# Optimization experiments

Measured on AMD Instinct MI355X. Metric: run time of the kernel, lower is better.

## Reference

```python
import jax, jax.numpy as jnp
import numpy as np

D = 768
OUT = 196
EPS = 1e-6


def setup_inputs() -> dict:
    key = jax.random.key(0)
    k_x, k_w, k_b, k_g, k_beta = jax.random.split(key, 5)
    x = jax.random.normal(k_x, (16, 4096, D), dtype=jnp.float32)
    # LayerNorm affine params
    gamma = jnp.ones((D,), dtype=jnp.float32) + 0.01 * jax.random.normal(k_g, (D,), dtype=jnp.float32)
    beta = 0.01 * jax.random.normal(k_beta, (D,), dtype=jnp.float32)
    # Linear params (torch default init: U(-1/sqrt(D), 1/sqrt(D)))
    bound = 1.0 / np.sqrt(D)
    W = jax.random.uniform(k_w, (OUT, D), minval=-bound, maxval=bound, dtype=jnp.float32)
    b = jax.random.uniform(k_b, (OUT,), minval=-bound, maxval=bound, dtype=jnp.float32)
    return {"x": x, "gamma": gamma, "beta": beta, "W": W, "b": b}


def reference(x, gamma, beta, W, b):
    # LayerNorm over last dim (768), eps=1e-6, elementwise affine
    mean = jnp.mean(x, axis=-1, keepdims=True)
    var = jnp.mean(jnp.square(x - mean), axis=-1, keepdims=True)
    xn = (x - mean) * jax.lax.rsqrt(var + EPS) * gamma + beta
    # Linear 768 -> 196
    return jnp.einsum('bsd,od->bso', xn, W) + b
```

## Files before the change

### kernel.cpp

```cpp
#include <hip/hip_runtime.h>

#define DD    768
#define OUTN  196
#define MT    16
#define KC    256
#define APAD  264
#define KTS   8

typedef __attribute__((ext_vector_type(8))) _Float16 halfx8;
typedef __attribute__((ext_vector_type(4))) _Float16 halfx4;
typedef __attribute__((ext_vector_type(4))) float    f32x4;

__global__ __launch_bounds__(256) void wprep_kernel(const float4* __restrict__ W4,
                                                    halfx4* __restrict__ Wh4) {
    int i = blockIdx.x * 256 + threadIdx.x;
    if (i < OUTN * DD / 4) {
        float4 v = W4[i];
        halfx4 h;
        h[0] = (_Float16)v.x; h[1] = (_Float16)v.y;
        h[2] = (_Float16)v.z; h[3] = (_Float16)v.w;
        Wh4[i] = h;
    }
}

__global__ __launch_bounds__(256, 4) void fused_ln_linear(
    const float* __restrict__ x, const float* __restrict__ gamma,
    const float* __restrict__ beta, const _Float16* __restrict__ Wh,
    const float* __restrict__ bias, float* __restrict__ out)
{
    __shared__ _Float16 Ahi[2][MT * APAD];
    __shared__ _Float16 Alo[2][MT * APAD];

    const int tid  = threadIdx.x;
    const int wv   = tid >> 6;
    const int lane = tid & 63;
    const long row0 = (long)blockIdx.x * MT;
    const float* xrow = x + (row0 + wv * 4) * DD + lane * 4;

    float mean[4], rstd[4];
    {
        float s[4], ss[4];
#pragma unroll
        for (int t = 0; t < 4; ++t) { s[t] = 0.f; ss[t] = 0.f; }
#pragma unroll
        for (int t = 0; t < 4; ++t) {
#pragma unroll
            for (int c = 0; c < 3; ++c) {
                const float4 v = *(const float4*)(xrow + t * DD + c * KC);
                s[t]  += v.x + v.y + v.z + v.w;
                ss[t] += v.x * v.x + v.y * v.y + v.z * v.z + v.w * v.w;
            }
        }
#pragma unroll
        for (int t = 0; t < 4; ++t) {
#pragma unroll
            for (int off = 32; off > 0; off >>= 1) {
                s[t]  += __shfl_xor(s[t],  off);
                ss[t] += __shfl_xor(ss[t], off);
            }
            mean[t] = s[t] * (1.f / DD);
            const float var = ss[t] * (1.f / DD) - mean[t] * mean[t];
            rstd[t] = rsqrtf(var + 1e-6f);
        }
    }

    const int cnt  = (wv == 0) ? 4 : 3;
    const int nt0  = (wv == 0) ? 0 : (1 + 3 * wv);
    const int ln16 = lane & 15;
    const int q    = lane >> 4;

    int ncol[4], nload[4];
    float bs[4];
#pragma unroll
    for (int i = 0; i < 4; ++i) {
        const int n = (nt0 + i) * 16 + ln16;
        ncol[i]  = n;
        nload[i] = (n < OUTN ? n : OUTN - 1) * DD;
        bs[i]    = (n < OUTN) ? bias[n] : 0.f;
    }

    f32x4 acc[4];
#pragma unroll
    for (int i = 0; i < 4; ++i) acc[i] = (f32x4){0.f, 0.f, 0.f, 0.f};

    auto stage_write = [&](int st, int buf) {
        const int k0 = st * KC + lane * 4;
        const float4 gv = *(const float4*)(gamma + k0);
        const float4 bv = *(const float4*)(beta + k0);
#pragma unroll
        for (int t = 0; t < 4; ++t) {
            const float4 v = *(const float4*)(xrow + t * DD + st * KC);
            const float y0 = (v.x - mean[t]) * rstd[t] * gv.x + bv.x;
            const float y1 = (v.y - mean[t]) * rstd[t] * gv.y + bv.y;
            const float y2 = (v.z - mean[t]) * rstd[t] * gv.z + bv.z;
            const float y3 = (v.w - mean[t]) * rstd[t] * gv.w + bv.w;
            halfx4 hi, lo;
            hi[0] = (_Float16)y0; lo[0] = (_Float16)(y0 - (float)hi[0]);
            hi[1] = (_Float16)y1; lo[1] = (_Float16)(y1 - (float)hi[1]);
            hi[2] = (_Float16)y2; lo[2] = (_Float16)(y2 - (float)hi[2]);
            hi[3] = (_Float16)y3; lo[3] = (_Float16)(y3 - (float)hi[3]);
            const int r = wv * 4 + t;
            *(halfx4*)(&Ahi[buf][r * APAD + lane * 4]) = hi;
            *(halfx4*)(&Alo[buf][r * APAD + lane * 4]) = lo;
        }
    };

    auto gemm_stage = [&](int st, int buf) {
        const _Float16* Aph = &Ahi[buf][ln16 * APAD + q * 8];
        const _Float16* Apl = &Alo[buf][ln16 * APAD + q * 8];
#pragma unroll
        for (int kt = 0; kt < KTS; ++kt) {
            const halfx8 ah = *(const halfx8*)(Aph + kt * 32);
            const halfx8 al = *(const halfx8*)(Apl + kt * 32);
#pragma unroll
            for (int i = 0; i < 4; ++i) {
                if (i < cnt) {
                    const halfx8 bf =
                        *(const halfx8*)(Wh + nload[i] + st * KC + kt * 32 + q * 8);
                    acc[i] = __builtin_amdgcn_mfma_f32_16x16x32_f16(ah, bf, acc[i], 0, 0, 0);
                    acc[i] = __builtin_amdgcn_mfma_f32_16x16x32_f16(al, bf, acc[i], 0, 0, 0);
                }
            }
        }
    };

    stage_write(0, 0);
    __syncthreads();

    stage_write(1, 1);
    gemm_stage(0, 0);
    __syncthreads();

    stage_write(2, 0);
    gemm_stage(1, 1);
    __syncthreads();

    gemm_stage(2, 0);

    const long rbase = row0 + q * 4;
#pragma unroll
    for (int i = 0; i < 4; ++i) {
        if (i < cnt && ncol[i] < OUTN) {
#pragma unroll
            for (int rg = 0; rg < 4; ++rg)
                out[(rbase + rg) * OUTN + ncol[i]] = acc[i][rg] + bs[i];
        }
    }
}

extern "C" void kernel_launch(void* const* d_in, const int* in_sizes, int n_in,
                              void* d_out, int out_size, void* d_ws, size_t ws_size,
                              hipStream_t stream) {
    const float* x     = (const float*)d_in[0];
    const float* gamma = (const float*)d_in[1];
    const float* beta  = (const float*)d_in[2];
    const float* W     = (const float*)d_in[3];
    const float* b     = (const float*)d_in[4];
    float* out = (float*)d_out;
    _Float16* Wh = (_Float16*)d_ws;

    wprep_kernel<<<(OUTN * DD / 4 + 255) / 256, 256, 0, stream>>>(
        (const float4*)W, (halfx4*)Wh);

    const long rows = 16L * 4096;
    fused_ln_linear<<<rows / MT, 256, 0, stream>>>(x, gamma, beta, Wh, b, out);
}
```

Before: 416.0 us.

## Fold LayerNorm affine into weights and apply normalization after GEMM

Gamma is folded into the fp16 weights, and beta·W plus the bias is precomputed into a per-output constant. The main kernel then multiplies raw x (split into hi/lo fp16) directly and applies mean/rstd as an epilogue correction using per-column weight sums. This removes the separate statistics pass, the LDS staging and the block barriers, and lets each wave own 16 rows across all 13 output tiles straight from registers. The cost is heavy register pressure from 13 accumulators. It also risks precision loss from cancellation in acc - mean*Ssum, and the weight sum is taken over fp16-rounded weights times fp32 x.

```diff
diff --git a/kernel.cpp b/kernel.cpp
--- a/kernel.cpp
+++ b/kernel.cpp
@@ -1,149 +1,119 @@
 #include <hip/hip_runtime.h>
 
-#define DD    768
-#define OUTN  196
-#define MT    16
-#define KC    256
-#define APAD  264
-#define KTS   8
+#define DD   768
+#define OUTN 196
+#define NT   13
+#define KT   24
 
 typedef __attribute__((ext_vector_type(8))) _Float16 halfx8;
-typedef __attribute__((ext_vector_type(4))) _Float16 halfx4;
 typedef __attribute__((ext_vector_type(4))) float    f32x4;
 
-__global__ __launch_bounds__(256) void wprep_kernel(const float4* __restrict__ W4,
-                                                    halfx4* __restrict__ Wh4) {
-    int i = blockIdx.x * 256 + threadIdx.x;
-    if (i < OUTN * DD / 4) {
-        float4 v = W4[i];
-        halfx4 h;
-        h[0] = (_Float16)v.x; h[1] = (_Float16)v.y;
-        h[2] = (_Float16)v.z; h[3] = (_Float16)v.w;
-        Wh4[i] = h;
+__global__ __launch_bounds__(256) void wprep_kernel(
+    const float* __restrict__ W, const float* __restrict__ gamma,
+    const float* __restrict__ beta, const float* __restrict__ bias,
+    _Float16* __restrict__ Wh, float* __restrict__ Ssum, float* __restrict__ cvec)
+{
+    __shared__ float red[2][4];
+    const int n   = blockIdx.x;
+    const int tid = threadIdx.x;
+    float s1 = 0.f, s2 = 0.f;
+#pragma unroll
+    for (int kk = 0; kk < 3; ++kk) {
+        const int k = tid + kk * 256;
+        const float w = W[n * DD + k];
+        const _Float16 h = (_Float16)(w * gamma[k]);
+        Wh[n * DD + k] = h;
+        s1 += (float)h;
+        s2 += beta[k] * w;
+    }
+#pragma unroll
+    for (int off = 32; off > 0; off >>= 1) {
+        s1 += __shfl_xor(s1, off);
+        s2 += __shfl_xor(s2, off);
+    }
+    if ((tid & 63) == 0) { red[0][tid >> 6] = s1; red[1][tid >> 6] = s2; }
+    __syncthreads();
+    if (tid == 0) {
+        Ssum[n] = red[0][0] + red[0][1] + red[0][2] + red[0][3];
+        cvec[n] = bias[n] + red[1][0] + red[1][1] + red[1][2] + red[1][3];
     }
 }
 
 __global__ __launch_bounds__(256, 4) void fused_ln_linear(
-    const float* __restrict__ x, const float* __restrict__ gamma,
-    const float* __restrict__ beta, const _Float16* __restrict__ Wh,
-    const float* __restrict__ bias, float* __restrict__ out)
+    const float* __restrict__ x, const _Float16* __restrict__ Wh,
+    const float* __restrict__ Ssum, const float* __restrict__ cvec,
+    float* __restrict__ out)
 {
-    __shared__ _Float16 Ahi[2][MT * APAD];
-    __shared__ _Float16 Alo[2][MT * APAD];
-
     const int tid  = threadIdx.x;
     const int wv   = tid >> 6;
     const int lane = tid & 63;
-    const long row0 = (long)blockIdx.x * MT;
-    const float* xrow = x + (row0 + wv * 4) * DD + lane * 4;
+    const int ln16 = lane & 15;
+    const int q    = lane >> 4;
 
-    float mean[4], rstd[4];
-    {
-        float s[4], ss[4];
+    const long row0 = (long)blockIdx.x * 64 + wv * 16;
+    const float* xp = x + (row0 + ln16) * DD + q * 8;
+
+    int woff[NT];
 #pragma unroll
-        for (int t = 0; t < 4; ++t) { s[t] = 0.f; ss[t] = 0.f; }
+    for (int nt = 0; nt < NT; ++nt) {
+        int n = nt * 16 + ln16;
+        if (n >= OUTN) n = OUTN - 1;
+        woff[nt] = n * DD + q * 8;
+    }
+
+    f32x4 acc[NT];
 #pragma unroll
-        for (int t = 0; t < 4; ++t) {
+    for (int i = 0; i < NT; ++i) acc[i] = (f32x4){0.f, 0.f, 0.f, 0.f};
+
+    float s = 0.f, ss = 0.f;
+
+#pragma unroll 2
+    for (int kt = 0; kt < KT; ++kt) {
+        const float4 v0 = *(const float4*)(xp + kt * 32);
+        const float4 v1 = *(const float4*)(xp + kt * 32 + 4);
+        s  += v0.x + v0.y + v0.z + v0.w + v1.x + v1.y + v1.z + v1.w;
+        ss += v0.x * v0.x + v0.y * v0.y + v0.z * v0.z + v0.w * v0.w
+            + v1.x * v1.x + v1.y * v1.y + v1.z * v1.z + v1.w * v1.w;
+        halfx8 hi, lo;
+        hi[0] = (_Float16)v0.x; lo[0] = (_Float16)(v0.x - (float)hi[0]);
+        hi[1] = (_Float16)v0.y; lo[1] = (_Float16)(v0.y - (float)hi[1]);
+        hi[2] = (_Float16)v0.z; lo[2] = (_Float16)(v0.z - (float)hi[2]);
+        hi[3] = (_Float16)v0.w; lo[3] = (_Float16)(v0.w - (float)hi[3]);
+        hi[4] = (_Float16)v1.x; lo[4] = (_Float16)(v1.x - (float)hi[4]);
+        hi[5] = (_Float16)v1.y; lo[5] = (_Float16)(v1.y - (float)hi[5]);
+        hi[6] = (_Float16)v1.z; lo[6] = (_Float16)(v1.z - (float)hi[6]);
+        hi[7] = (_Float16)v1.w; lo[7] = (_Float16)(v1.w - (float)hi[7]);
 #pragma unroll
-            for (int c = 0; c < 3; ++c) {
-                const float4 v = *(const float4*)(xrow + t * DD + c * KC);
-                s[t]  += v.x + v.y + v.z + v.w;
-                ss[t] += v.x * v.x + v.y * v.y + v.z * v.z + v.w * v.w;
-            }
-        }
-#pragma unroll
-        for (int t = 0; t < 4; ++t) {
-#pragma unroll
-            for (int off = 32; off > 0; off >>= 1) {
-                s[t]  += __shfl_xor(s[t],  off);
-                ss[t] += __shfl_xor(ss[t], off);
-            }
-            mean[t] = s[t] * (1.f / DD);
-            const float var = ss[t] * (1.f / DD) - mean[t] * mean[t];
-            rstd[t] = rsqrtf(var + 1e-6f);
+        for (int nt = 0; nt < NT; ++nt) {
+            const halfx8 bw = *(const halfx8*)(Wh + woff[nt] + kt * 32);
+            acc[nt] = __builtin_amdgcn_mfma_f32_16x16x32_f16(hi, bw, acc[nt], 0, 0, 0);
+            acc[nt] = __builtin_amdgcn_mfma_f32_16x16x32_f16(lo, bw, acc[nt], 0, 0, 0);
         }
     }
 
-    const int cnt  = (wv == 0) ? 4 : 3;
-    const int nt0  = (wv == 0) ? 0 : (1 + 3 * wv);
-    const int ln16 = lane & 15;
-    const int q    = lane >> 4;
+    s  += __shfl_xor(s, 16);  s  += __shfl_xor(s, 32);
+    ss += __shfl_xor(ss, 16); ss += __shfl_xor(ss, 32);
+    const float mean_r = s * (1.f / DD);
+    const float rstd_r = rsqrtf(ss * (1.f / DD) - mean_r * mean_r + 1e-6f);
 
-    int ncol[4], nload[4];
-    float bs[4];
+    float mb[4], rb[4];
 #pragma unroll
-    for (int i = 0; i < 4; ++i) {
-        const int n = (nt0 + i) * 16 + ln16;
-        ncol[i]  = n;
-        nload[i] = (n < OUTN ? n : OUTN - 1) * DD;
-        bs[i]    = (n < OUTN) ? bias[n] : 0.f;
+    for (int rg = 0; rg < 4; ++rg) {
+        const int src = q * 4 + rg;
+        mb[rg] = __shfl(mean_r, src);
+        rb[rg] = __shfl(rstd_r, src);
     }
 
-    f32x4 acc[4];
+    const long obase = (row0 + q * 4) * OUTN;
 #pragma unroll
-    for (int i = 0; i < 4; ++i) acc[i] = (f32x4){0.f, 0.f, 0.f, 0.f};
-
-    auto stage_write = [&](int st, int buf) {
-        const int k0 = st * KC + lane * 4;
-        const float4 gv = *(const float4*)(gamma + k0);
-        const float4 bv = *(const float4*)(beta + k0);
-#pragma unroll
-        for (int t = 0; t < 4; ++t) {
-            const float4 v = *(const float4*)(xrow + t * DD + st * KC);
-            const float y0 = (v.x - mean[t]) * rstd[t] * gv.x + bv.x;
-            const float y1 = (v.y - mean[t]) * rstd[t] * gv.y + bv.y;
-            const float y2 = (v.z - mean[t]) * rstd[t] * gv.z + bv.z;
-            const float y3 = (v.w - mean[t]) * rstd[t] * gv.w + bv.w;
-            halfx4 hi, lo;
-            hi[0] = (_Float16)y0; lo[0] = (_Float16)(y0 - (float)hi[0]);
-            hi[1] = (_Float16)y1; lo[1] = (_Float16)(y1 - (float)hi[1]);
-            hi[2] = (_Float16)y2; lo[2] = (_Float16)(y2 - (float)hi[2]);
-            hi[3] = (_Float16)y3; lo[3] = (_Float16)(y3 - (float)hi[3]);
-            const int r = wv * 4 + t;
-            *(halfx4*)(&Ahi[buf][r * APAD + lane * 4]) = hi;
-            *(halfx4*)(&Alo[buf][r * APAD + lane * 4]) = lo;
-        }
-    };
-
-    auto gemm_stage = [&](int st, int buf) {
-        const _Float16* Aph = &Ahi[buf][ln16 * APAD + q * 8];
-        const _Float16* Apl = &Alo[buf][ln16 * APAD + q * 8];
-#pragma unroll
-        for (int kt = 0; kt < KTS; ++kt) {
-            const halfx8 ah = *(const halfx8*)(Aph + kt * 32);
-            const halfx8 al = *(const halfx8*)(Apl + kt * 32);
-#pragma unroll
-            for (int i = 0; i < 4; ++i) {
-                if (i < cnt) {
-                    const halfx8 bf =
-                        *(const halfx8*)(Wh + nload[i] + st * KC + kt * 32 + q * 8);
-                    acc[i] = __builtin_amdgcn_mfma_f32_16x16x32_f16(ah, bf, acc[i], 0, 0, 0);
-                    acc[i] = __builtin_amdgcn_mfma_f32_16x16x32_f16(al, bf, acc[i], 0, 0, 0);
-                }
-            }
-        }
-    };
-
-    stage_write(0, 0);
-    __syncthreads();
-
-    stage_write(1, 1);
-    gemm_stage(0, 0);
-    __syncthreads();
-
-    stage_write(2, 0);
-    gemm_stage(1, 1);
-    __syncthreads();
-
-    gemm_stage(2, 0);
-
-    const long rbase = row0 + q * 4;
-#pragma unroll
-    for (int i = 0; i < 4; ++i) {
-        if (i < cnt && ncol[i] < OUTN) {
+    for (int nt = 0; nt < NT; ++nt) {
+        const int n = nt * 16 + ln16;
+        if (n < OUTN) {
+            const float Sp = Ssum[n];
+            const float cn = cvec[n];
 #pragma unroll
             for (int rg = 0; rg < 4; ++rg)
-                out[(rbase + rg) * OUTN + ncol[i]] = acc[i][rg] + bs[i];
+                out[obase + rg * OUTN + n] = rb[rg] * (acc[nt][rg] - mb[rg] * Sp) + cn;
         }
     }
 }
@@ -157,11 +127,13 @@
     const float* W     = (const float*)d_in[3];
     const float* b     = (const float*)d_in[4];
     float* out = (float*)d_out;
-    _Float16* Wh = (_Float16*)d_ws;
 
-    wprep_kernel<<<(OUTN * DD / 4 + 255) / 256, 256, 0, stream>>>(
-        (const float4*)W, (halfx4*)Wh);
+    _Float16* Wh  = (_Float16*)d_ws;
+    float*    Ss  = (float*)((char*)d_ws + OUTN * DD * sizeof(_Float16));
+    float*    cv  = Ss + OUTN;
+
+    wprep_kernel<<<OUTN, 256, 0, stream>>>(W, gamma, beta, b, Wh, Ss, cv);
 
     const long rows = 16L * 4096;
-    fused_ln_linear<<<rows / MT, 256, 0, stream>>>(x, gamma, beta, Wh, b, out);
+    fused_ln_linear<<<rows / 64, 256, 0, stream>>>(x, Wh, Ss, cv, out);
 }
```

Measured after the change: 414.9 us. Within noise of the previous version (-0.3%).
